# Kernel tuning notes

Measured on AMD Instinct MI355X. Metric: run time of the kernel, lower is better.

The kernel has to match this reference:

```python
import jax, jax.numpy as jnp
import numpy as np

B, T, C, H = 4, 2048, 1024, 16
D = C // H  # head dim 64


def setup_inputs() -> dict:
    key = jax.random.key(0)
    ks = jax.random.split(key, 5)
    s = 1.0 / np.sqrt(C)
    return {
        "x": jax.random.normal(ks[0], (B, T, C), jnp.float32),
        "Wq": jax.random.normal(ks[1], (C, C), jnp.float32) * s,
        "bq": jnp.zeros((C,), jnp.float32),
        "Wk": jax.random.normal(ks[2], (C, C), jnp.float32) * s,
        "bk": jnp.zeros((C,), jnp.float32),
        "Wv": jax.random.normal(ks[3], (C, C), jnp.float32) * s,
        "bv": jnp.zeros((C,), jnp.float32),
        "Wp": jax.random.normal(ks[4], (C, C), jnp.float32) * s,
        "bp": jnp.zeros((C,), jnp.float32),
    }


def reference(x, Wq, bq, Wk, bk, Wv, bv, Wp, bp):
    # project and split heads: [B,T,C] -> [B,H,T,D]
    def heads(w, b):
        return (x @ w.T + b).reshape(B, T, H, D).transpose(0, 2, 1, 3)

    q = heads(Wq, bq)
    k = heads(Wk, bk)
    v = heads(Wv, bv)

    att = jnp.einsum("bhqd,bhkd->bhqk", q, k) * (1.0 / np.sqrt(D))
    causal = jnp.tril(jnp.ones((T, T), bool))  # [T,T]
    att = jnp.where(causal[None, None], att, -jnp.inf)
    att = jax.nn.softmax(att, axis=-1)
    # dropout prob is 0.0 -> identity
    y = jnp.einsum("bhqk,bhkd->bhqd", att, v)
    y = y.transpose(0, 2, 1, 3).reshape(B, T, C)
    return y @ Wp.T + bp
```

## Files before the change

kernel.cpp:

```cpp
#include <hip/hip_runtime.h>
#include <hip/hip_bf16.h>

#define BB 4
#define TT 2048
#define CC 1024
#define HH 16
#define DD 64
#define PSTR 72

typedef unsigned short u16;
typedef __attribute__((ext_vector_type(8))) short bf16x8;
typedef __attribute__((ext_vector_type(4))) float f32x4;
typedef __attribute__((ext_vector_type(16))) float f32x16;

__device__ __forceinline__ float bf2f(u16 v) {
    union { unsigned u; float f; } c; c.u = ((unsigned)v) << 16; return c.f;
}
__device__ __forceinline__ u16 f2bf(float f) {
    union { float f; unsigned u; } c; c.f = f;
    unsigned u = c.u + 0x7fffu + ((c.u >> 16) & 1u);
    return (u16)(u >> 16);
}
__device__ __forceinline__ float fast_exp2(float x) {
    float r;
    asm volatile("v_exp_f32 %0, %1\n\ts_nop 1" : "=v"(r) : "v"(x));
    return r;
}
__device__ __forceinline__ unsigned pack_bf16(unsigned b0, unsigned b1) {
    unsigned d;
    asm("v_perm_b32 %0, %1, %2, %3" : "=v"(d) : "v"(b1), "v"(b0), "v"(0x07060302u));
    return d;
}
__device__ __forceinline__ uint2 pack4(float v0, float v1, float v2, float v3) {
    uint2 pk;
    pk.x = pack_bf16(__float_as_uint(v0) + 0x8000u, __float_as_uint(v1) + 0x8000u);
    pk.y = pack_bf16(__float_as_uint(v2) + 0x8000u, __float_as_uint(v3) + 0x8000u);
    return pk;
}
__device__ __forceinline__ unsigned cvtpk_bf16(float lo, float hi) {
    unsigned r;
    asm("v_cvt_pk_bf16_f32 %0, %1, %2" : "=v"(r) : "v"(lo), "v"(hi));
    return r;
}
__device__ __forceinline__ void gload16(const u16* g, u16* l) {
    __builtin_amdgcn_global_load_lds(
        (const __attribute__((address_space(1))) void*)g,
        (__attribute__((address_space(3))) void*)l, 16, 0, 0);
}

__device__ __forceinline__ int detect_bf16(const u16* __restrict__ xprobe, int* sh) {
    const int t = threadIdx.x;
    u16 hh = xprobe[2 * t];
    int e = (hh >> 7) & 0xFF;
    unsigned long long m = __ballot(e >= 118 && e <= 132);
    if ((t & 63) == 0) sh[t >> 6] = __popcll(m);
    __syncthreads();
    return (sh[0] + sh[1] + sh[2] + sh[3]) >= 128;
}

struct CastArgs {
    const void* src[9];
    u16* dst[9];
    int blk_start[10];
    int n[9];
};
__global__ __launch_bounds__(256) void cast_all(CastArgs a, const u16* __restrict__ xprobe) {
    __shared__ int sh[4];
    const int isbf = detect_bf16(xprobe, sh);
    int b = blockIdx.x;
    int s = 0;
    while (s < 8 && b >= a.blk_start[s + 1]) s++;
    int i0 = (b - a.blk_start[s]) * 2048 + threadIdx.x * 8;
    if (i0 + 8 > a.n[s]) return;
    if (isbf) {
        *(uint4*)&a.dst[s][i0] = *(const uint4*)&((const u16*)a.src[s])[i0];
    } else {
        const float* sp = (const float*)a.src[s];
        u16 tmp[8];
#pragma unroll
        for (int j = 0; j < 8; j++) tmp[j] = f2bf(sp[i0 + j]);
        *(uint4*)&a.dst[s][i0] = *(uint4*)tmp;
    }
}

__device__ __forceinline__ void gemm_core(
    const u16* __restrict__ X, const u16* __restrict__ W,
    u16* Als, u16* Bls, f32x16 (&acc)[2][2],
    int m0, int n0, int wave, int lane, int wm, int wn)
{
    const int l32 = lane & 31;
    const int hv  = lane >> 5;
    int srow[4], sch[4];
#pragma unroll
    for (int c = 0; c < 4; c++) {
        srow[c] = wave * 32 + c * 8 + (lane >> 3);
        sch[c]  = (lane & 7) ^ (srow[c] & 7);
    }

    for (int k0 = 0; k0 < CC; k0 += 64) {
        __syncthreads();
#pragma unroll
        for (int c = 0; c < 4; c++) {
            gload16(&X[(size_t)(m0 + srow[c]) * CC + k0 + sch[c] * 8],
                    &Als[wave * 2048 + c * 512]);
            gload16(&W[(size_t)(n0 + srow[c]) * CC + k0 + sch[c] * 8],
                    &Bls[wave * 2048 + c * 512]);
        }
        __syncthreads();

#pragma unroll
        for (int ks = 0; ks < 4; ks++) {
            const int sw = ((ks * 2 + hv) ^ (l32 & 7)) * 8;
            bf16x8 a[2], b[2];
#pragma unroll
            for (int i = 0; i < 2; i++)
                a[i] = *(const bf16x8*)&Als[(wm + i * 32 + l32) * 64 + sw];
#pragma unroll
            for (int j = 0; j < 2; j++)
                b[j] = *(const bf16x8*)&Bls[(wn + j * 32 + l32) * 64 + sw];
#pragma unroll
            for (int i = 0; i < 2; i++)
#pragma unroll
                for (int j = 0; j < 2; j++)
                    acc[i][j] = __builtin_amdgcn_mfma_f32_32x32x16_bf16(
                        b[j], a[i], acc[i][j], 0, 0, 0);
        }
    }
}

__global__ __launch_bounds__(256, 2) void gemm_qkv(
    const u16* __restrict__ X,
    const u16* __restrict__ Wq, const u16* __restrict__ Wk, const u16* __restrict__ Wv,
    const u16* __restrict__ bq, const u16* __restrict__ bk, const u16* __restrict__ bv,
    u16* __restrict__ Q, u16* __restrict__ K, u16* __restrict__ VT)
{
    __shared__ __align__(16) u16 Als[128 * 64];
    __shared__ __align__(16) u16 Bls[3 * 128 * 64];

    const int tid  = threadIdx.x;
    const int wave = tid >> 6;
    const int lane = tid & 63;
    const int l32  = lane & 31;
    const int hv   = lane >> 5;
    const int m0   = blockIdx.x * 128;
    const int n0   = blockIdx.y * 128;
    const int wm   = (wave >> 1) * 64;
    const int wn   = (wave & 1) * 64;

    const u16* Ws[3]  = {Wq, Wk, Wv};

    f32x16 acc[3][2][2];
#pragma unroll
    for (int z = 0; z < 3; z++)
#pragma unroll
        for (int i = 0; i < 2; i++)
#pragma unroll
            for (int j = 0; j < 2; j++) acc[z][i][j] = (f32x16)0.0f;

    int srow[4], sch[4];
#pragma unroll
    for (int c = 0; c < 4; c++) {
        srow[c] = wave * 32 + c * 8 + (lane >> 3);
        sch[c]  = (lane & 7) ^ (srow[c] & 7);
    }

    for (int k0 = 0; k0 < CC; k0 += 64) {
        __syncthreads();
#pragma unroll
        for (int c = 0; c < 4; c++)
            gload16(&X[(size_t)(m0 + srow[c]) * CC + k0 + sch[c] * 8],
                    &Als[wave * 2048 + c * 512]);
#pragma unroll
        for (int z = 0; z < 3; z++)
#pragma unroll
            for (int c = 0; c < 4; c++)
                gload16(&Ws[z][(size_t)(n0 + srow[c]) * CC + k0 + sch[c] * 8],
                        &Bls[z * 8192 + wave * 2048 + c * 512]);
        __syncthreads();

#pragma unroll
        for (int ks = 0; ks < 4; ks++) {
            const int sw = ((ks * 2 + hv) ^ (l32 & 7)) * 8;
            bf16x8 a[2];
#pragma unroll
            for (int i = 0; i < 2; i++)
                a[i] = *(const bf16x8*)&Als[(wm + i * 32 + l32) * 64 + sw];
#pragma unroll
            for (int z = 0; z < 3; z++) {
                bf16x8 b[2];
#pragma unroll
                for (int j = 0; j < 2; j++)
                    b[j] = *(const bf16x8*)&Bls[z * 8192 + (wn + j * 32 + l32) * 64 + sw];
#pragma unroll
                for (int i = 0; i < 2; i++)
#pragma unroll
                    for (int j = 0; j < 2; j++)
                        acc[z][i][j] = __builtin_amdgcn_mfma_f32_32x32x16_bf16(
                            b[j], a[i], acc[z][i][j], 0, 0, 0);
            }
        }
    }

    const u16* biases[3] = {bq, bk, bv};
    u16* outs[3]         = {Q, K, VT};

#pragma unroll
    for (int z = 0; z < 3; z++) {
        const float scale = (z == 0) ? 0.18033688f : 1.0f;
        const u16* bias = biases[z];
        u16* outp = outs[z];
#pragma unroll
        for (int j = 0; j < 2; j++) {
#pragma unroll
            for (int rq = 0; rq < 4; rq++) {
                const int n_base = n0 + wn + j * 32 + rq * 8 + hv * 4;
                union { uint2 u; u16 us[4]; } braw;
                braw.u = *(const uint2*)&bias[n_base];
                const int hh = n_base >> 6, d0 = n_base & 63;
#pragma unroll
                for (int i = 0; i < 2; i++) {
                    const int m = m0 + wm + i * 32 + l32;
                    const int bb = m >> 11, t = m & (TT - 1);
                    float v0 = (acc[z][i][j][rq * 4 + 0] + bf2f(braw.us[0])) * scale;
                    float v1 = (acc[z][i][j][rq * 4 + 1] + bf2f(braw.us[1])) * scale;
                    float v2 = (acc[z][i][j][rq * 4 + 2] + bf2f(braw.us[2])) * scale;
                    float v3 = (acc[z][i][j][rq * 4 + 3] + bf2f(braw.us[3])) * scale;
                    if (z < 2) {
                        *(uint2*)&outp[((size_t)(bb * HH + hh) * TT + t) * DD + d0] =
                            pack4(v0, v1, v2, v3);
                    } else {
                        const size_t base = (size_t)(bb * HH + hh) * DD * TT + t;
                        outp[base + (size_t)(d0 + 0) * TT] = f2bf(v0);
                        outp[base + (size_t)(d0 + 1) * TT] = f2bf(v1);
                        outp[base + (size_t)(d0 + 2) * TT] = f2bf(v2);
                        outp[base + (size_t)(d0 + 3) * TT] = f2bf(v3);
                    }
                }
            }
        }
    }
}

__global__ __launch_bounds__(256, 4) void gemm_proj(
    const u16* __restrict__ X, const u16* __restrict__ W,
    const u16* __restrict__ bias, void* __restrict__ out,
    const u16* __restrict__ xprobe)
{
    __shared__ __align__(16) u16 Als[128 * 64];
    __shared__ __align__(16) u16 Bls[128 * 64];
    __shared__ int sh[4];

    const int isbf = detect_bf16(xprobe, sh);

    const int tid  = threadIdx.x;
    const int wave = tid >> 6;
    const int lane = tid & 63;
    const int l32  = lane & 31;
    const int hv   = lane >> 5;
    const int m0   = blockIdx.x * 128;
    const int n0   = blockIdx.y * 128;
    const int wm   = (wave >> 1) * 64;
    const int wn   = (wave & 1) * 64;

    f32x16 acc[2][2];
#pragma unroll
    for (int i = 0; i < 2; i++)
#pragma unroll
        for (int j = 0; j < 2; j++) acc[i][j] = (f32x16)0.0f;

    gemm_core(X, W, Als, Bls, acc, m0, n0, wave, lane, wm, wn);

#pragma unroll
    for (int j = 0; j < 2; j++) {
#pragma unroll
        for (int rq = 0; rq < 4; rq++) {
            const int n_base = n0 + wn + j * 32 + rq * 8 + hv * 4;
            union { uint2 u; u16 us[4]; } braw;
            braw.u = *(const uint2*)&bias[n_base];
#pragma unroll
            for (int i = 0; i < 2; i++) {
                const int m = m0 + wm + i * 32 + l32;
                float v0 = acc[i][j][rq * 4 + 0] + bf2f(braw.us[0]);
                float v1 = acc[i][j][rq * 4 + 1] + bf2f(braw.us[1]);
                float v2 = acc[i][j][rq * 4 + 2] + bf2f(braw.us[2]);
                float v3 = acc[i][j][rq * 4 + 3] + bf2f(braw.us[3]);
                if (isbf) {
                    *(uint2*)&((u16*)out)[(size_t)m * CC + n_base] = pack4(v0, v1, v2, v3);
                } else {
                    float4 f; f.x = v0; f.y = v1; f.z = v2; f.w = v3;
                    *(float4*)&((float*)out)[(size_t)m * CC + n_base] = f;
                }
            }
        }
    }
}

__global__ __launch_bounds__(256, 3) void attn_kernel(
    const u16* __restrict__ Qg, const u16* __restrict__ Kg,
    const u16* __restrict__ VTg, u16* __restrict__ Yg)
{
    __shared__ __align__(16) u16 Ks[2][64 * 64];
    __shared__ __align__(16) u16 VTs[2][64 * 64];
    __shared__ __align__(16) u16 Ps[128 * PSTR];
    __shared__ float ls[128];

    const int tid  = threadIdx.x;
    const int wave = tid >> 6;
    const int lane = tid & 63;
    const int quad = lane >> 4;
    const int l16  = lane & 15;
    const int ly   = (l16 & 7) ^ (l16 >> 3);
    const int bh    = blockIdx.x;
    const int qtile = (TT / 128 - 1) - blockIdx.y;
    const int h = bh & (HH - 1);
    const int b = bh >> 4;
    const int q0 = qtile * 128;

    bf16x8 qf[2][2];
#pragma unroll
    for (int g = 0; g < 2; g++)
#pragma unroll
        for (int ks = 0; ks < 2; ks++)
            qf[g][ks] = *(const bf16x8*)&Qg[((size_t)bh * TT + q0 + wave * 32 +
                                             g * 16 + l16) * DD + ks * 32 + quad * 8];

    const u16* kp[2];
    const u16* vp[2];
#pragma unroll
    for (int c = 0; c < 2; c++) {
        const int srow = wave * 16 + c * 8 + (lane >> 3);
        const int sch  = (lane & 7) ^ (lane >> 3) ^ ((wave * 2 + c) & 7);
        kp[c] = Kg + (size_t)bh * TT * DD + (size_t)srow * DD + sch * 8;
        vp[c] = VTg + (size_t)bh * DD * TT + (size_t)srow * TT + sch * 8;
    }

    f32x4 o_acc[2][4];
#pragma unroll
    for (int g = 0; g < 2; g++)
#pragma unroll
        for (int jt = 0; jt < 4; jt++) o_acc[g][jt] = (f32x4)0.0f;
    float lsum[2] = {0.0f, 0.0f};

    const int ntiles = 2 * qtile;
    const int nkv    = ntiles + 2;

#pragma unroll
    for (int c = 0; c < 2; c++) {
        gload16(kp[c], &Ks[0][wave * 1024 + c * 512]);
        gload16(vp[c], &VTs[0][wave * 1024 + c * 512]);
        kp[c] += 64 * DD;
        vp[c] += 64;
    }

    for (int kv = 0; kv < nkv; kv++) {
        const bool masked = (kv >= ntiles);
        const int cur = kv & 1;
        __syncthreads();
        if (kv + 1 < nkv) {
#pragma unroll
            for (int c = 0; c < 2; c++) {
                gload16(kp[c], &Ks[cur ^ 1][wave * 1024 + c * 512]);
                gload16(vp[c], &VTs[cur ^ 1][wave * 1024 + c * 512]);
                kp[c] += 64 * DD;
                vp[c] += 64;
            }
        }

        f32x4 st[2][4];
#pragma unroll
        for (int g = 0; g < 2; g++)
#pragma unroll
            for (int j = 0; j < 4; j++) st[g][j] = (f32x4)0.0f;
        __builtin_amdgcn_s_setprio(1);
#pragma unroll
        for (int ks = 0; ks < 2; ks++) {
            const int rsw = ((ks * 4 + quad) ^ ly) * 8;
#pragma unroll
            for (int j = 0; j < 4; j++) {
                bf16x8 kf = *(const bf16x8*)&Ks[cur][(j * 16 + l16) * 64 + (rsw ^ (j * 16))];
#pragma unroll
                for (int g = 0; g < 2; g++)
                    st[g][j] = __builtin_amdgcn_mfma_f32_16x16x32_bf16(
                        kf, qf[g][ks], st[g][j], 0, 0, 0);
            }
        }
        __builtin_amdgcn_s_setprio(0);

#pragma unroll
        for (int g = 0; g < 2; g++) {
            u16* psrow = &Ps[(wave * 32 + g * 16 + l16) * PSTR];
            const int qrow = q0 + wave * 32 + g * 16 + l16;
            float lp = 0.0f;
#pragma unroll
            for (int j = 0; j < 4; j++) {
                float e0 = fast_exp2(st[g][j][0]);
                float e1 = fast_exp2(st[g][j][1]);
                float e2 = fast_exp2(st[g][j][2]);
                float e3 = fast_exp2(st[g][j][3]);
                if (masked) {
                    const int kc = kv * 64 + j * 16 + quad * 4;
                    if (kc + 0 > qrow) e0 = 0.0f;
                    if (kc + 1 > qrow) e1 = 0.0f;
                    if (kc + 2 > qrow) e2 = 0.0f;
                    if (kc + 3 > qrow) e3 = 0.0f;
                }
                lp += (e0 + e1) + (e2 + e3);
                uint2 pk;
                pk.x = cvtpk_bf16(e0, e1);
                pk.y = cvtpk_bf16(e2, e3);
                *(uint2*)&psrow[j * 16 + quad * 4] = pk;
            }
            lsum[g] += lp;
        }

        __builtin_amdgcn_s_setprio(1);
#pragma unroll
        for (int ks = 0; ks < 2; ks++) {
            const int rsw = ((ks * 4 + quad) ^ ly) * 8;
            bf16x8 vfk[4];
#pragma unroll
            for (int jt = 0; jt < 4; jt++)
                vfk[jt] = *(const bf16x8*)&VTs[cur][(jt * 16 + l16) * 64 + (rsw ^ (jt * 16))];
#pragma unroll
            for (int g = 0; g < 2; g++) {
                bf16x8 pf = *(const bf16x8*)&Ps[(wave * 32 + g * 16 + l16) * PSTR +
                                                ks * 32 + quad * 8];
#pragma unroll
                for (int jt = 0; jt < 4; jt++)
                    o_acc[g][jt] = __builtin_amdgcn_mfma_f32_16x16x32_bf16(
                        pf, vfk[jt], o_acc[g][jt], 0, 0, 0);
            }
        }
        __builtin_amdgcn_s_setprio(0);
    }

#pragma unroll
    for (int g = 0; g < 2; g++) {
        lsum[g] += __shfl_xor(lsum[g], 16, 64);
        lsum[g] += __shfl_xor(lsum[g], 32, 64);
        ls[wave * 32 + g * 16 + l16] = lsum[g];
    }

#pragma unroll
    for (int g = 0; g < 2; g++) {
        float linv[4];
#pragma unroll
        for (int r = 0; r < 4; r++)
            linv[r] = 1.0f / fmaxf(ls[wave * 32 + g * 16 + quad * 4 + r], 1e-20f);
#pragma unroll
        for (int jt = 0; jt < 4; jt++) {
#pragma unroll
            for (int r = 0; r < 4; r++) {
                const int t = q0 + wave * 32 + g * 16 + quad * 4 + r;
                const int c = h * DD + jt * 16 + l16;
                Yg[((size_t)b * TT + t) * CC + c] = f2bf(o_acc[g][jt][r] * linv[r]);
            }
        }
    }
}

extern "C" void kernel_launch(void* const* d_in, const int* in_sizes, int n_in,
                              void* d_out, int out_size, void* d_ws, size_t ws_size,
                              hipStream_t stream) {
    u16* w = (u16*)d_ws;
    size_t off = 0;
    const size_t NX = (size_t)BB * TT * CC;
    const size_t NW = (size_t)CC * CC;
    const size_t NB = CC;
    const size_t per = (size_t)BB * HH * TT * DD;

    u16* xb  = w + off; off += NX;
    u16* Wqb = w + off; off += NW;
    u16* Wkb = w + off; off += NW;
    u16* Wvb = w + off; off += NW;
    u16* Wpb = w + off; off += NW;
    u16* bqb = w + off; off += NB;
    u16* bkb = w + off; off += NB;
    u16* bvb = w + off; off += NB;
    u16* bpb = w + off; off += NB;
    u16* Q   = w + off; off += per;
    u16* K   = w + off; off += per;
    u16* VT  = w + off; off += per;
    u16* Y   = w + off; off += per;

    CastArgs ca;
    const int srcmap[9] = {0, 1, 3, 5, 7, 2, 4, 6, 8};
    u16* dsts[9] = {xb, Wqb, Wkb, Wvb, Wpb, bqb, bkb, bvb, bpb};
    int ns[9] = {(int)NX, (int)NW, (int)NW, (int)NW, (int)NW,
                 (int)NB, (int)NB, (int)NB, (int)NB};
    int acc_blk = 0;
    for (int i = 0; i < 9; i++) {
        ca.src[i] = d_in[srcmap[i]];
        ca.dst[i] = dsts[i];
        ca.n[i]   = ns[i];
        ca.blk_start[i] = acc_blk;
        acc_blk += (ns[i] + 2047) / 2048;
    }
    ca.blk_start[9] = acc_blk;
    cast_all<<<acc_blk, 256, 0, stream>>>(ca, (const u16*)d_in[0]);

    gemm_qkv<<<dim3(64, 8), 256, 0, stream>>>(xb, Wqb, Wkb, Wvb,
                                              bqb, bkb, bvb, Q, K, VT);
    attn_kernel<<<dim3(BB * HH, TT / 128), 256, 0, stream>>>(Q, K, VT, Y);
    gemm_proj<<<dim3(64, 8), 256, 0, stream>>>(Y, Wpb, bpb, d_out,
                                               (const u16*)d_in[0]);
}
```

Measured before the change: 247.0 us.

## Enlarge attention query tile to 256 rows with 8 waves per block

```diff
diff --git a/kernel.cpp b/kernel.cpp
--- a/kernel.cpp
+++ b/kernel.cpp
@@ -295,14 +295,14 @@
     }
 }
 
-__global__ __launch_bounds__(256, 3) void attn_kernel(
+__global__ __launch_bounds__(512, 4) void attn_kernel(
     const u16* __restrict__ Qg, const u16* __restrict__ Kg,
     const u16* __restrict__ VTg, u16* __restrict__ Yg)
 {
     __shared__ __align__(16) u16 Ks[2][64 * 64];
     __shared__ __align__(16) u16 VTs[2][64 * 64];
-    __shared__ __align__(16) u16 Ps[128 * PSTR];
-    __shared__ float ls[128];
+    __shared__ __align__(16) u16 Ps[256 * PSTR];
+    __shared__ float ls[256];
 
     const int tid  = threadIdx.x;
     const int wave = tid >> 6;
@@ -310,11 +310,11 @@
     const int quad = lane >> 4;
     const int l16  = lane & 15;
     const int ly   = (l16 & 7) ^ (l16 >> 3);
-    const int bh    = blockIdx.x;
-    const int qtile = (TT / 128 - 1) - blockIdx.y;
+    const int bh   = blockIdx.x;
+    const int qblk = (TT / 256 - 1) - blockIdx.y;
     const int h = bh & (HH - 1);
     const int b = bh >> 4;
-    const int q0 = qtile * 128;
+    const int q0 = qblk * 256;
 
     bf16x8 qf[2][2];
 #pragma unroll
@@ -324,15 +324,10 @@
             qf[g][ks] = *(const bf16x8*)&Qg[((size_t)bh * TT + q0 + wave * 32 +
                                              g * 16 + l16) * DD + ks * 32 + quad * 8];
 
-    const u16* kp[2];
-    const u16* vp[2];
-#pragma unroll
-    for (int c = 0; c < 2; c++) {
-        const int srow = wave * 16 + c * 8 + (lane >> 3);
-        const int sch  = (lane & 7) ^ (lane >> 3) ^ ((wave * 2 + c) & 7);
-        kp[c] = Kg + (size_t)bh * TT * DD + (size_t)srow * DD + sch * 8;
-        vp[c] = VTg + (size_t)bh * DD * TT + (size_t)srow * TT + sch * 8;
-    }
+    const int srow = wave * 8 + (lane >> 3);
+    const int sch  = (lane & 7) ^ (lane >> 3) ^ (wave & 7);
+    const u16* kp = Kg + (size_t)bh * TT * DD + (size_t)srow * DD + sch * 8;
+    const u16* vp = VTg + (size_t)bh * DD * TT + (size_t)srow * TT + sch * 8;
 
     f32x4 o_acc[2][4];
 #pragma unroll
@@ -341,29 +336,22 @@
         for (int jt = 0; jt < 4; jt++) o_acc[g][jt] = (f32x4)0.0f;
     float lsum[2] = {0.0f, 0.0f};
 
-    const int ntiles = 2 * qtile;
-    const int nkv    = ntiles + 2;
-
-#pragma unroll
-    for (int c = 0; c < 2; c++) {
-        gload16(kp[c], &Ks[0][wave * 1024 + c * 512]);
-        gload16(vp[c], &VTs[0][wave * 1024 + c * 512]);
-        kp[c] += 64 * DD;
-        vp[c] += 64;
-    }
-
-    for (int kv = 0; kv < nkv; kv++) {
-        const bool masked = (kv >= ntiles);
+    const int nt = qblk * 4 + 4;
+
+    gload16(kp, &Ks[0][wave * 512]);
+    gload16(vp, &VTs[0][wave * 512]);
+    kp += 64 * DD;
+    vp += 64;
+
+    for (int kv = 0; kv < nt; kv++) {
+        const bool masked = (kv >= nt - 4);
         const int cur = kv & 1;
         __syncthreads();
-        if (kv + 1 < nkv) {
-#pragma unroll
-            for (int c = 0; c < 2; c++) {
-                gload16(kp[c], &Ks[cur ^ 1][wave * 1024 + c * 512]);
-                gload16(vp[c], &VTs[cur ^ 1][wave * 1024 + c * 512]);
-                kp[c] += 64 * DD;
-                vp[c] += 64;
-            }
+        if (kv + 1 < nt) {
+            gload16(kp, &Ks[cur ^ 1][wave * 512]);
+            gload16(vp, &VTs[cur ^ 1][wave * 512]);
+            kp += 64 * DD;
+            vp += 64;
         }
 
         f32x4 st[2][4];
@@ -501,7 +489,7 @@
 
     gemm_qkv<<<dim3(64, 8), 256, 0, stream>>>(xb, Wqb, Wkb, Wvb,
                                               bqb, bkb, bvb, Q, K, VT);
-    attn_kernel<<<dim3(BB * HH, TT / 128), 256, 0, stream>>>(Q, K, VT, Y);
+    attn_kernel<<<dim3(BB * HH, TT / 256), 512, 0, stream>>>(Q, K, VT, Y);
     gemm_proj<<<dim3(64, 8), 256, 0, stream>>>(Y, Wpb, bpb, d_out,
                                                (const u16*)d_in[0]);
 }
```

Result: slower. 252.0 us (+2.0%).
